# Kernel tuning notes

Measured on AMD Instinct MI355X. Metric: run time of the kernel, lower is better.

## Reference

```python
import jax, jax.numpy as jnp
import numpy as np

# Dims: C cells, L gene tokens, E embed, H mlp hidden, M factors, K topk
C, L, E, H, M, K = 16, 8192, 512, 256, 128, 30
TAU = 1.0        # gumbel-softmax temperature
SOFTNESS = 0.01  # soft-mask sharpness
TEMP = 1.0       # logits temperature
EPS = 1e-20


def setup_inputs() -> dict:
    key = jax.random.key(0)
    ks = jax.random.split(key, 7)
    x = jax.random.normal(ks[0], (C, L, E), dtype=jnp.float32)
    key_padding_mask = jax.random.randint(ks[1], (C, L), 0, 2) > 0  # True = valid
    uniform_noise = jax.random.uniform(ks[2], (C, L - 1, M), dtype=jnp.float32)
    W1 = jax.random.normal(ks[3], (E, H), dtype=jnp.float32) * (1.0 / np.sqrt(E))
    b1 = jnp.zeros((H,), dtype=jnp.float32)
    W2 = jax.random.normal(ks[4], (H, M), dtype=jnp.float32) * (1.0 / np.sqrt(H))
    b2 = jnp.zeros((M,), dtype=jnp.float32)
    return {"x": x, "key_padding_mask": key_padding_mask,
            "uniform_noise": uniform_noise,
            "W1": W1, "b1": b1, "W2": W2, "b2": b2}


def reference(x, key_padding_mask, uniform_noise, W1, b1, W2, b2):
    # default gene_subset: drop token 0, keep the rest  -> S = L-1
    xs = x[:, 1:, :]                          # (C, S, E)
    kpm = key_padding_mask[:, 1:]             # (C, S)

    # 2-layer MLP router (dropout p=0 -> identity)
    h = jax.nn.relu(jnp.einsum('cse,eh->csh', xs, W1) + b1)   # (C, S, H)
    logits = (jnp.einsum('csh,hm->csm', h, W2) + b2) / TEMP    # (C, S, M)

    # GumbelTopK, training path: gumbel-softmax then smooth top-k mask
    gumbel = -jnp.log(-jnp.log(uniform_noise + EPS) + EPS)
    perturbed = (logits + gumbel) / TAU
    probs = jax.nn.softmax(perturbed, axis=-1)                 # (C, S, M)
    topk_vals, _ = jax.lax.top_k(probs, K)                     # (C, S, K)
    threshold = topk_vals[..., -1:]                            # (C, S, 1)
    smooth_mask = jax.nn.sigmoid((probs - threshold) / SOFTNESS)
    out = probs * smooth_mask

    # faithful to the source: mask = ~key_padding_mask; probs *= mask
    out = out * (~kpm)[..., None].astype(out.dtype)
    return out, kpm
```

## Files before the change

### kernel.cpp

```cpp
#include <hip/hip_runtime.h>
#include <hip/hip_bf16.h>

#define CC 16
#define LL 8192
#define SS 8191
#define EE 512
#define HH 256
#define MM 128
#define TOPK 30
#define TOT (CC * SS)

typedef __attribute__((ext_vector_type(8))) short short8;
typedef __attribute__((ext_vector_type(4))) float f32x4;
typedef __attribute__((ext_vector_type(4))) unsigned int u32x4;

static __device__ __forceinline__ unsigned short f2bf(float f) {
    unsigned u = __builtin_bit_cast(unsigned, f);
    u += 0x7FFFu + ((u >> 16) & 1u);
    return (unsigned short)(u >> 16);
}

static __device__ __forceinline__ unsigned pk2(float lo, float hi) {
    __hip_bfloat162 t = __float22bfloat162_rn(float2{lo, hi});
    unsigned u;
    __builtin_memcpy(&u, &t, 4);
    return u;
}

static __device__ __forceinline__ short8 cvt8(const float4 a, const float4 b) {
    u32x4 uv;
    uv[0] = pk2(a.x, a.y);
    uv[1] = pk2(a.z, a.w);
    uv[2] = pk2(b.x, b.y);
    uv[3] = pk2(b.z, b.w);
    return __builtin_bit_cast(short8, uv);
}

static __device__ __forceinline__ void gl2lds16(const float* g, unsigned char* l) {
    __builtin_amdgcn_global_load_lds(
        (const __attribute__((address_space(1))) void*)g,
        (__attribute__((address_space(3))) void*)l,
        16, 0, 0);
}

template<int CTRL>
static __device__ __forceinline__ float dppf(float v) {
    return __builtin_bit_cast(float,
        __builtin_amdgcn_update_dpp(0, __builtin_bit_cast(int, v), CTRL, 0xF, 0xF, false));
}
template<int CTRL>
static __device__ __forceinline__ int dppi(int v) {
    return __builtin_amdgcn_update_dpp(0, v, CTRL, 0xF, 0xF, false);
}
static __device__ __forceinline__ float sum16f(float v) {
    v += dppf<0x121>(v); v += dppf<0x122>(v); v += dppf<0x124>(v); v += dppf<0x128>(v);
    return v;
}
static __device__ __forceinline__ float max16f(float v) {
    v = fmaxf(v, dppf<0x121>(v)); v = fmaxf(v, dppf<0x122>(v));
    v = fmaxf(v, dppf<0x124>(v)); v = fmaxf(v, dppf<0x128>(v));
    return v;
}
static __device__ __forceinline__ unsigned sum16u(unsigned v) {
    v += (unsigned)dppi<0x121>((int)v); v += (unsigned)dppi<0x122>((int)v);
    v += (unsigned)dppi<0x124>((int)v); v += (unsigned)dppi<0x128>((int)v);
    return v;
}

__global__ void prep_weights(const float* __restrict__ W1, const float* __restrict__ W2,
                             unsigned short* __restrict__ W1T, unsigned short* __restrict__ W2T)
{
    const int b = blockIdx.x, tid = threadIdx.x;
    if (b < 64) {
        const int e0 = b * 8, h = tid;
        short8 sv;
#pragma unroll
        for (int j = 0; j < 8; ++j)
            sv[j] = (short)f2bf(W1[(size_t)(e0 + j) * HH + h]);
        *(short8*)(void*)(W1T + (size_t)h * EE + e0) = sv;
    } else {
        const int h0 = (b - 64) * 16;
        if (tid < MM) {
            const int m = tid;
            short8 s0v, s1v;
#pragma unroll
            for (int j = 0; j < 8; ++j) {
                s0v[j] = (short)f2bf(W2[(size_t)(h0 + j) * MM + m]);
                s1v[j] = (short)f2bf(W2[(size_t)(h0 + 8 + j) * MM + m]);
            }
            *(short8*)(void*)(W2T + (size_t)m * HH + h0) = s0v;
            *(short8*)(void*)(W2T + (size_t)m * HH + h0 + 8) = s1v;
        }
    }
}

__global__ __launch_bounds__(512, 4)
void gene_gemm_kernel(const float* __restrict__ x,
                      const unsigned short* __restrict__ W1T,
                      const float* __restrict__ b1,
                      const unsigned short* __restrict__ W2T,
                      float* __restrict__ logits)
{
    __shared__ __align__(16) unsigned char lds[65536];

    const int tid = threadIdx.x;
    const int c   = blockIdx.y;
    const int s0  = blockIdx.x * 128;

    const int w    = tid >> 6;
    const int lane = tid & 63;
    const int lr   = lane & 15;
    const int kq   = lane >> 4;
    const int wr   = w >> 2;
    const int wc   = w & 3;
    const int tx   = tid & 15;
    const int ty   = tid >> 4;

    const float* xb = x + ((size_t)c * LL + s0 + 1) * EE;

#define STAGE(ck, bufoff) do {                                              \
    _Pragma("unroll")                                                       \
    for (int it_ = 0; it_ < 4; ++it_) {                                     \
        const int row_ = it_ * 32 + ty;                                     \
        const int rs_  = min(s0 + row_, SS - 1) - s0;                       \
        const float* g_ = xb + (size_t)rs_ * EE + (ck) * 64                 \
                          + ((tx ^ (row_ & 7)) << 2);                       \
        gl2lds16(g_, lds + (bufoff) + (it_ * 512 + tid) * 16);              \
    } } while (0)

    const int cw = wc * 64;
    float b1v[4];
#pragma unroll
    for (int n = 0; n < 4; ++n) b1v[n] = b1[cw + n * 16 + lr];

    f32x4 acc[4][4];
#pragma unroll
    for (int r = 0; r < 4; ++r)
#pragma unroll
        for (int n = 0; n < 4; ++n) acc[r][n] = (f32x4)0.0f;

    STAGE(0, 0);
    __syncthreads();

    for (int ck = 0; ck < 8; ++ck) {
        const int cur = (ck & 1) << 15;
        if (ck < 7) STAGE(ck + 1, ((ck + 1) & 1) << 15);
#pragma unroll
        for (int ks = 0; ks < 2; ++ks) {
            short8 af[4];
#pragma unroll
            for (int r = 0; r < 4; ++r) {
                const int row = wr * 64 + r * 16 + lr;
                const int ug  = ks * 8 + kq * 2;
                const float4 a0 = *(const float4*)(const void*)
                    (lds + cur + row * 256 + (((ug + 0) ^ (row & 7)) << 4));
                const float4 a1 = *(const float4*)(const void*)
                    (lds + cur + row * 256 + (((ug + 1) ^ (row & 7)) << 4));
                af[r] = cvt8(a0, a1);
            }
            short8 bf_[4];
#pragma unroll
            for (int n = 0; n < 4; ++n)
                bf_[n] = *(const short8*)(const void*)
                    (W1T + (size_t)(cw + n * 16 + lr) * EE + ck * 64 + ks * 32 + kq * 8);
#pragma unroll
            for (int r = 0; r < 4; ++r)
#pragma unroll
                for (int n = 0; n < 4; ++n)
                    acc[r][n] = __builtin_amdgcn_mfma_f32_16x16x32_bf16(af[r], bf_[n], acc[r][n], 0, 0, 0);
        }
        __syncthreads();
    }

#pragma unroll
    for (int n = 0; n < 4; ++n) {
        const int colh = cw + n * 16 + lr;
#pragma unroll
        for (int r = 0; r < 4; ++r)
#pragma unroll
            for (int q = 0; q < 4; ++q) {
                const int row = wr * 64 + r * 16 + kq * 4 + q;
                *(unsigned short*)(lds + row * 512 + ((colh * 2) ^ ((row & 7) << 4))) =
                    f2bf(fmaxf(acc[r][n][q] + b1v[n], 0.0f));
            }
    }
    __syncthreads();

    f32x4 acc2[4][2];
#pragma unroll
    for (int r = 0; r < 4; ++r)
#pragma unroll
        for (int n = 0; n < 2; ++n) acc2[r][n] = (f32x4)0.0f;

    const int cw2 = wc * 32;
#pragma unroll 4
    for (int ks = 0; ks < 8; ++ks) {
        short8 ah[4];
#pragma unroll
        for (int r = 0; r < 4; ++r) {
            const int row = wr * 64 + r * 16 + lr;
            ah[r] = *(const short8*)(const void*)
                (lds + row * 512 + ((ks * 64 + kq * 16) ^ ((row & 7) << 4)));
        }
        short8 bw[2];
#pragma unroll
        for (int n = 0; n < 2; ++n)
            bw[n] = *(const short8*)(const void*)
                (W2T + (size_t)(cw2 + n * 16 + lr) * HH + ks * 32 + kq * 8);
#pragma unroll
        for (int r = 0; r < 4; ++r)
#pragma unroll
            for (int n = 0; n < 2; ++n)
                acc2[r][n] = __builtin_amdgcn_mfma_f32_16x16x32_bf16(ah[r], bw[n], acc2[r][n], 0, 0, 0);
    }

#pragma unroll
    for (int r = 0; r < 4; ++r)
#pragma unroll
        for (int n = 0; n < 2; ++n)
#pragma unroll
            for (int q = 0; q < 4; ++q) {
                const int s = s0 + wr * 64 + r * 16 + kq * 4 + q;
                if (s < SS)
                    logits[((size_t)c * SS + s) * MM + cw2 + n * 16 + lr] = acc2[r][n][q];
            }
#undef STAGE
}

__global__ __launch_bounds__(256, 8)
void gene_epi_kernel(const float* __restrict__ noise,
                     const int*   __restrict__ mask,
                     const float* __restrict__ b2,
                     float* __restrict__ out,
                     float* __restrict__ outk)
{
    const int tid = threadIdx.x;
    const int tx  = tid & 15;
    const int ty  = tid >> 4;
    const long base = (long)blockIdx.x * 64;

    if (tid < 64) {
        const long gr = base + tid;
        if (gr < TOT) {
            const int cc2 = (int)(gr / SS);
            outk[gr] = (mask[gr + cc2 + 1] != 0) ? 1.0f : 0.0f;
        }
    }

    float b2v[8];
    {
        const float4 bb0 = *(const float4*)(b2 + tx * 8 + 0);
        const float4 bb1 = *(const float4*)(b2 + tx * 8 + 4);
        b2v[0]=bb0.x; b2v[1]=bb0.y; b2v[2]=bb0.z; b2v[3]=bb0.w;
        b2v[4]=bb1.x; b2v[5]=bb1.y; b2v[6]=bb1.z; b2v[7]=bb1.w;
    }

    float pr[4][8];
    float pmaxv[4];
    float mz[4];
    long  grv[4];

#pragma unroll
    for (int i = 0; i < 4; ++i) {
        const long gr  = base + ty * 4 + i;
        grv[i] = gr;
        const long grc = gr < TOT ? gr : (TOT - 1);
        const int  cc2 = (int)(grc / SS);
        mz[i] = (mask[grc + cc2 + 1] != 0) ? 0.0f : 1.0f;

        const float* lp = out   + grc * MM + tx * 8;
        const float* np = noise + grc * MM + tx * 8;
        const float4 l0 = *(const float4*)lp;
        const float4 l1 = *(const float4*)(lp + 4);
        const float4 u0 = *(const float4*)np;
        const float4 u1 = *(const float4*)(np + 4);
        const float lg[8] = {l0.x,l0.y,l0.z,l0.w,l1.x,l1.y,l1.z,l1.w};
        const float uu[8] = {u0.x,u0.y,u0.z,u0.w,u1.x,u1.y,u1.z,u1.w};
        float pm[8];
#pragma unroll
        for (int q = 0; q < 8; ++q) {
            const float g = -__logf(-__logf(uu[q] + 1e-20f) + 1e-20f);
            pm[q] = lg[q] + b2v[q] + g;
        }
        float mx = pm[0];
#pragma unroll
        for (int q = 1; q < 8; ++q) mx = fmaxf(mx, pm[q]);
        mx = max16f(mx);
        float se = 0.0f;
#pragma unroll
        for (int q = 0; q < 8; ++q) { pr[i][q] = __expf(pm[q] - mx); se += pr[i][q]; }
        se = sum16f(se);
        const float inv = 1.0f / se;
#pragma unroll
        for (int q = 0; q < 8; ++q) pr[i][q] *= inv;
        pmaxv[i] = inv;
    }

    float lo[4], hi[4];
#pragma unroll
    for (int i = 0; i < 4; ++i) { lo[i] = 0.0f; hi[i] = fminf(pmaxv[i], 1.0f / 30.0f); }
    for (int it = 0; it < 10; ++it) {
        float mid[4];
#pragma unroll
        for (int i = 0; i < 4; ++i) mid[i] = 0.5f * (lo[i] + hi[i]);
        unsigned cnt = 0;
#pragma unroll
        for (int q = 0; q < 8; ++q) {
            cnt += (pr[0][q] > mid[0]) ? 1u : 0u;
            cnt += (pr[1][q] > mid[1]) ? (1u << 8) : 0u;
            cnt += (pr[2][q] > mid[2]) ? (1u << 16) : 0u;
            cnt += (pr[3][q] > mid[3]) ? (1u << 24) : 0u;
        }
        cnt = sum16u(cnt);
#pragma unroll
        for (int i = 0; i < 4; ++i) {
            const bool ge = ((cnt >> (8 * i)) & 255u) >= TOPK;
            lo[i] = ge ? mid[i] : lo[i];
            hi[i] = ge ? hi[i] : mid[i];
        }
    }

#pragma unroll
    for (int i = 0; i < 4; ++i) {
        if (grv[i] < TOT) {
            float ov[8];
#pragma unroll
            for (int q = 0; q < 8; ++q) {
                const float sm = 1.0f / (1.0f + __expf((hi[i] - pr[i][q]) * 100.0f));
                ov[q] = pr[i][q] * sm * mz[i];
            }
            float* op = out + grv[i] * MM + tx * 8;
            float4 o0, o1;
            o0.x=ov[0]; o0.y=ov[1]; o0.z=ov[2]; o0.w=ov[3];
            o1.x=ov[4]; o1.y=ov[5]; o1.z=ov[6]; o1.w=ov[7];
            *(float4*)(op + 0) = o0;
            *(float4*)(op + 4) = o1;
        }
    }
}

extern "C" void kernel_launch(void* const* d_in, const int* in_sizes, int n_in,
                              void* d_out, int out_size, void* d_ws, size_t ws_size,
                              hipStream_t stream) {
    const float* x     = (const float*)d_in[0];
    const int*   mask  = (const int*)d_in[1];
    const float* noise = (const float*)d_in[2];
    const float* W1    = (const float*)d_in[3];
    const float* b1    = (const float*)d_in[4];
    const float* W2    = (const float*)d_in[5];
    const float* b2    = (const float*)d_in[6];
    float* out  = (float*)d_out;
    float* outk = out + (size_t)CC * SS * MM;

    unsigned short* W1T = (unsigned short*)d_ws;
    unsigned short* W2T = W1T + (size_t)HH * EE;

    prep_weights<<<dim3(80), dim3(256), 0, stream>>>(W1, W2, W1T, W2T);

    gene_gemm_kernel<<<dim3(64, CC), dim3(512), 0, stream>>>(x, W1T, b1, W2T, out);

    const int nblk = (TOT + 63) / 64;
    gene_epi_kernel<<<dim3(nblk), dim3(256), 0, stream>>>(noise, mask, b2, out, outk);
}
```

Measured before the change: 177.1 us.

## Deepen GEMM1 x-tile pipeline to four stages with register-prefetched W1

Cuts the first GEMM's K chunks from 64 to 32 floats and rotates four LDS buffers with three chunks in flight. Waits on a partial vmcnt instead of a full __syncthreads each chunk. W1 fragments are double-buffered in registers and prefetched one chunk ahead. The goal is to hide global-load latency behind MFMA work. Correctness now depends on hand-counted vmcnt values and on the compiler not reordering the sched_barrier regions.

Measured after the change: 232.5 us. 1.31x slower.

```diff
diff --git a/kernel.cpp b/kernel.cpp
--- a/kernel.cpp
+++ b/kernel.cpp
@@ -113,22 +113,29 @@
     const int kq   = lane >> 4;
     const int wr   = w >> 2;
     const int wc   = w & 3;
-    const int tx   = tid & 15;
-    const int ty   = tid >> 4;
 
     const float* xb = x + ((size_t)c * LL + s0 + 1) * EE;
-
-#define STAGE(ck, bufoff) do {                                              \
+    const int cw = wc * 64;
+
+#define STAGE(ck) do {                                                      \
+    const int bo_ = ((ck) & 3) * 16384;                                     \
     _Pragma("unroll")                                                       \
-    for (int it_ = 0; it_ < 4; ++it_) {                                     \
-        const int row_ = it_ * 32 + ty;                                     \
+    for (int j_ = 0; j_ < 2; ++j_) {                                        \
+        const int unit_ = j_ * 512 + tid;                                   \
+        const int row_ = unit_ >> 3, uu_ = unit_ & 7;                       \
         const int rs_  = min(s0 + row_, SS - 1) - s0;                       \
-        const float* g_ = xb + (size_t)rs_ * EE + (ck) * 64                 \
-                          + ((tx ^ (row_ & 7)) << 2);                       \
-        gl2lds16(g_, lds + (bufoff) + (it_ * 512 + tid) * 16);              \
+        const float* g_ = xb + (size_t)rs_ * EE + (ck) * 32                 \
+                          + ((uu_ ^ (row_ & 7)) << 2);                      \
+        gl2lds16(g_, lds + bo_ + unit_ * 16);                               \
     } } while (0)
 
-    const int cw = wc * 64;
+#define LOADW(dst, ck) do {                                                 \
+    _Pragma("unroll")                                                       \
+    for (int n_ = 0; n_ < 4; ++n_)                                          \
+        dst[n_] = *(const short8*)(const void*)                             \
+            (W1T + (size_t)(cw + n_ * 16 + lr) * EE + (ck) * 32 + kq * 8);  \
+    } while (0)
+
     float b1v[4];
 #pragma unroll
     for (int n = 0; n < 4; ++n) b1v[n] = b1[cw + n * 16 + lr];
@@ -139,38 +146,49 @@
 #pragma unroll
         for (int n = 0; n < 4; ++n) acc[r][n] = (f32x4)0.0f;
 
-    STAGE(0, 0);
+    short8 wA[4], wB[4];
+
+    LOADW(wA, 0);
+    STAGE(0); STAGE(1); STAGE(2);
+
+#define DO_CHUNK(C, V, WCUR, WNXT) do {                                     \
+    if ((C) < 15) LOADW(WNXT, (C) + 1);                                     \
+    __builtin_amdgcn_sched_barrier(0);                                      \
+    asm volatile("s_waitcnt vmcnt(" #V ")" ::: "memory");                   \
+    asm volatile("s_waitcnt lgkmcnt(0)" ::: "memory");                      \
+    __builtin_amdgcn_sched_barrier(0);                                      \
+    __builtin_amdgcn_s_barrier();                                           \
+    __builtin_amdgcn_sched_barrier(0);                                      \
+    if ((C) <= 12) STAGE((C) + 3);                                          \
+    const unsigned char* cb_ = lds + ((C) & 3) * 16384;                     \
+    short8 af_[4];                                                          \
+    _Pragma("unroll")                                                       \
+    for (int r_ = 0; r_ < 4; ++r_) {                                        \
+        const int row_ = wr * 64 + r_ * 16 + lr;                            \
+        const float4 a0_ = *(const float4*)(const void*)                    \
+            (cb_ + row_ * 128 + (((kq * 2 + 0) ^ (row_ & 7)) << 4));        \
+        const float4 a1_ = *(const float4*)(const void*)                    \
+            (cb_ + row_ * 128 + (((kq * 2 + 1) ^ (row_ & 7)) << 4));        \
+        af_[r_] = cvt8(a0_, a1_);                                           \
+    }                                                                       \
+    _Pragma("unroll")                                                       \
+    for (int r_ = 0; r_ < 4; ++r_)                                          \
+        _Pragma("unroll")                                                   \
+        for (int n_ = 0; n_ < 4; ++n_)                                      \
+            acc[r_][n_] = __builtin_amdgcn_mfma_f32_16x16x32_bf16(          \
+                af_[r_], WCUR[n_], acc[r_][n_], 0, 0, 0);                   \
+    } while (0)
+
+    DO_CHUNK( 0, 12, wA, wB); DO_CHUNK( 1, 16, wB, wA);
+    DO_CHUNK( 2, 20, wA, wB); DO_CHUNK( 3, 20, wB, wA);
+    DO_CHUNK( 4, 20, wA, wB); DO_CHUNK( 5, 20, wB, wA);
+    DO_CHUNK( 6, 20, wA, wB); DO_CHUNK( 7, 20, wB, wA);
+    DO_CHUNK( 8, 20, wA, wB); DO_CHUNK( 9, 20, wB, wA);
+    DO_CHUNK(10, 20, wA, wB); DO_CHUNK(11, 20, wB, wA);
+    DO_CHUNK(12, 20, wA, wB); DO_CHUNK(13, 20, wB, wA);
+    DO_CHUNK(14, 16, wA, wB); DO_CHUNK(15,  8, wB, wA);
+
     __syncthreads();
-
-    for (int ck = 0; ck < 8; ++ck) {
-        const int cur = (ck & 1) << 15;
-        if (ck < 7) STAGE(ck + 1, ((ck + 1) & 1) << 15);
-#pragma unroll
-        for (int ks = 0; ks < 2; ++ks) {
-            short8 af[4];
-#pragma unroll
-            for (int r = 0; r < 4; ++r) {
-                const int row = wr * 64 + r * 16 + lr;
-                const int ug  = ks * 8 + kq * 2;
-                const float4 a0 = *(const float4*)(const void*)
-                    (lds + cur + row * 256 + (((ug + 0) ^ (row & 7)) << 4));
-                const float4 a1 = *(const float4*)(const void*)
-                    (lds + cur + row * 256 + (((ug + 1) ^ (row & 7)) << 4));
-                af[r] = cvt8(a0, a1);
-            }
-            short8 bf_[4];
-#pragma unroll
-            for (int n = 0; n < 4; ++n)
-                bf_[n] = *(const short8*)(const void*)
-                    (W1T + (size_t)(cw + n * 16 + lr) * EE + ck * 64 + ks * 32 + kq * 8);
-#pragma unroll
-            for (int r = 0; r < 4; ++r)
-#pragma unroll
-                for (int n = 0; n < 4; ++n)
-                    acc[r][n] = __builtin_amdgcn_mfma_f32_16x16x32_bf16(af[r], bf_[n], acc[r][n], 0, 0, 0);
-        }
-        __syncthreads();
-    }
 
 #pragma unroll
     for (int n = 0; n < 4; ++n) {
@@ -224,6 +242,8 @@
                 if (s < SS)
                     logits[((size_t)c * SS + s) * MM + cw2 + n * 16 + lr] = acc2[r][n][q];
             }
+#undef DO_CHUNK
+#undef LOADW
 #undef STAGE
 }
 
```

## Shrink GEMM tile to 64 rows with single-buffered LDS for higher occupancy

Applied to the files above, without the earlier changes.

The fused MLP GEMM kernel now uses 64-row tiles, 256 threads and a 32 KB single LDS buffer, replacing 128-row tiles, 512 threads and a 64 KB double buffer. The x tile is staged in 128-wide K chunks with a sync before compute, so the explicit prefetch pipeline is gone. The intent is to fit more resident blocks per CU and launch twice as many blocks, hiding global-load latency through occupancy rather than software double buffering. In exchange, each W1T/W2T fragment is reused across fewer rows, so weight traffic roughly doubles, and loads and MFMA work within a block no longer overlap.

After: 368.6 us. 2.08x slower.

```diff
diff --git a/kernel.cpp b/kernel.cpp
--- a/kernel.cpp
+++ b/kernel.cpp
@@ -94,41 +94,27 @@
     }
 }
 
-__global__ __launch_bounds__(512, 4)
+__global__ __launch_bounds__(256, 5)
 void gene_gemm_kernel(const float* __restrict__ x,
                       const unsigned short* __restrict__ W1T,
                       const float* __restrict__ b1,
                       const unsigned short* __restrict__ W2T,
                       float* __restrict__ logits)
 {
-    __shared__ __align__(16) unsigned char lds[65536];
+    __shared__ __align__(16) unsigned char lds[32768];
 
     const int tid = threadIdx.x;
     const int c   = blockIdx.y;
-    const int s0  = blockIdx.x * 128;
+    const int s0  = blockIdx.x * 64;
 
     const int w    = tid >> 6;
     const int lane = tid & 63;
     const int lr   = lane & 15;
     const int kq   = lane >> 4;
-    const int wr   = w >> 2;
-    const int wc   = w & 3;
-    const int tx   = tid & 15;
-    const int ty   = tid >> 4;
 
     const float* xb = x + ((size_t)c * LL + s0 + 1) * EE;
-
-#define STAGE(ck, bufoff) do {                                              \
-    _Pragma("unroll")                                                       \
-    for (int it_ = 0; it_ < 4; ++it_) {                                     \
-        const int row_ = it_ * 32 + ty;                                     \
-        const int rs_  = min(s0 + row_, SS - 1) - s0;                       \
-        const float* g_ = xb + (size_t)rs_ * EE + (ck) * 64                 \
-                          + ((tx ^ (row_ & 7)) << 2);                       \
-        gl2lds16(g_, lds + (bufoff) + (it_ * 512 + tid) * 16);              \
-    } } while (0)
-
-    const int cw = wc * 64;
+    const int cw = w * 64;
+
     float b1v[4];
 #pragma unroll
     for (int n = 0; n < 4; ++n) b1v[n] = b1[cw + n * 16 + lr];
@@ -139,30 +125,36 @@
 #pragma unroll
         for (int n = 0; n < 4; ++n) acc[r][n] = (f32x4)0.0f;
 
-    STAGE(0, 0);
-    __syncthreads();
-
-    for (int ck = 0; ck < 8; ++ck) {
-        const int cur = (ck & 1) << 15;
-        if (ck < 7) STAGE(ck + 1, ((ck + 1) & 1) << 15);
-#pragma unroll
-        for (int ks = 0; ks < 2; ++ks) {
+#pragma unroll
+    for (int ck = 0; ck < 4; ++ck) {
+#pragma unroll
+        for (int j = 0; j < 8; ++j) {
+            const int unit = j * 256 + tid;
+            const int row = unit >> 5, uu = unit & 31;
+            const int rs = min(s0 + row, SS - 1) - s0;
+            const float* g = xb + (size_t)rs * EE + ck * 128 + ((uu ^ (row & 7)) << 2);
+            gl2lds16(g, lds + unit * 16);
+        }
+        __syncthreads();
+
+#pragma unroll
+        for (int ks = 0; ks < 4; ++ks) {
             short8 af[4];
 #pragma unroll
             for (int r = 0; r < 4; ++r) {
-                const int row = wr * 64 + r * 16 + lr;
-                const int ug  = ks * 8 + kq * 2;
+                const int row = r * 16 + lr;
+                const int u0 = ks * 8 + kq * 2;
                 const float4 a0 = *(const float4*)(const void*)
-                    (lds + cur + row * 256 + (((ug + 0) ^ (row & 7)) << 4));
+                    (lds + row * 512 + (((u0 + 0) ^ (row & 7)) << 4));
                 const float4 a1 = *(const float4*)(const void*)
-                    (lds + cur + row * 256 + (((ug + 1) ^ (row & 7)) << 4));
+                    (lds + row * 512 + (((u0 + 1) ^ (row & 7)) << 4));
                 af[r] = cvt8(a0, a1);
             }
             short8 bf_[4];
 #pragma unroll
             for (int n = 0; n < 4; ++n)
                 bf_[n] = *(const short8*)(const void*)
-                    (W1T + (size_t)(cw + n * 16 + lr) * EE + ck * 64 + ks * 32 + kq * 8);
+                    (W1T + (size_t)(cw + n * 16 + lr) * EE + ck * 128 + ks * 32 + kq * 8);
 #pragma unroll
             for (int r = 0; r < 4; ++r)
 #pragma unroll
@@ -179,7 +171,7 @@
         for (int r = 0; r < 4; ++r)
 #pragma unroll
             for (int q = 0; q < 4; ++q) {
-                const int row = wr * 64 + r * 16 + kq * 4 + q;
+                const int row = r * 16 + kq * 4 + q;
                 *(unsigned short*)(lds + row * 512 + ((colh * 2) ^ ((row & 7) << 4))) =
                     f2bf(fmaxf(acc[r][n][q] + b1v[n], 0.0f));
             }
@@ -192,13 +184,13 @@
 #pragma unroll
         for (int n = 0; n < 2; ++n) acc2[r][n] = (f32x4)0.0f;
 
-    const int cw2 = wc * 32;
+    const int cw2 = w * 32;
 #pragma unroll 4
     for (int ks = 0; ks < 8; ++ks) {
         short8 ah[4];
 #pragma unroll
         for (int r = 0; r < 4; ++r) {
-            const int row = wr * 64 + r * 16 + lr;
+            const int row = r * 16 + lr;
             ah[r] = *(const short8*)(const void*)
                 (lds + row * 512 + ((ks * 64 + kq * 16) ^ ((row & 7) << 4)));
         }
@@ -220,11 +212,10 @@
         for (int n = 0; n < 2; ++n)
 #pragma unroll
             for (int q = 0; q < 4; ++q) {
-                const int s = s0 + wr * 64 + r * 16 + kq * 4 + q;
+                const int s = s0 + r * 16 + kq * 4 + q;
                 if (s < SS)
                     logits[((size_t)c * SS + s) * MM + cw2 + n * 16 + lr] = acc2[r][n][q];
             }
-#undef STAGE
 }
 
 __global__ __launch_bounds__(256, 8)
@@ -357,7 +348,7 @@
 
     prep_weights<<<dim3(80), dim3(256), 0, stream>>>(W1, W2, W1T, W2T);
 
-    gene_gemm_kernel<<<dim3(64, CC), dim3(512), 0, stream>>>(x, W1T, b1, W2T, out);
+    gene_gemm_kernel<<<dim3(128, CC), dim3(256), 0, stream>>>(x, W1T, b1, W2T, out);
 
     const int nblk = (TOT + 63) / 64;
     gene_epi_kernel<<<dim3(nblk), dim3(256), 0, stream>>>(noise, mask, b2, out, outk);
```

## Stage x via registers with bf16 conversion before LDS write

Applied to the files above, without the earlier changes.

The GEMM kernel no longer uses direct global-to-LDS fp32 loads. Each thread now loads x rows into registers, converts them to bf16 once and writes them to a half-size swizzled LDS buffer. MFMA operand reads then load bf16 directly from LDS instead of converting fp32 per wave, and the loads for the next chunk are issued before the barrier so they overlap compute. Barriers are replaced by a custom lgkmcnt wait plus s_barrier. The trade-off is more register pressure and global latency now sitting in the register path, in exchange for less LDS traffic and no repeated conversions.

After: 181.0 us. 1.02x slower.

```diff
diff --git a/kernel.cpp b/kernel.cpp
--- a/kernel.cpp
+++ b/kernel.cpp
@@ -36,13 +36,6 @@
     return __builtin_bit_cast(short8, uv);
 }
 
-static __device__ __forceinline__ void gl2lds16(const float* g, unsigned char* l) {
-    __builtin_amdgcn_global_load_lds(
-        (const __attribute__((address_space(1))) void*)g,
-        (__attribute__((address_space(3))) void*)l,
-        16, 0, 0);
-}
-
 template<int CTRL>
 static __device__ __forceinline__ float dppf(float v) {
     return __builtin_bit_cast(float,
@@ -65,6 +58,13 @@
     v += (unsigned)dppi<0x121>((int)v); v += (unsigned)dppi<0x122>((int)v);
     v += (unsigned)dppi<0x124>((int)v); v += (unsigned)dppi<0x128>((int)v);
     return v;
+}
+
+static __device__ __forceinline__ void bar_lgkm() {
+    asm volatile("s_waitcnt lgkmcnt(0)" ::: "memory");
+    __builtin_amdgcn_sched_barrier(0);
+    __builtin_amdgcn_s_barrier();
+    __builtin_amdgcn_sched_barrier(0);
 }
 
 __global__ void prep_weights(const float* __restrict__ W1, const float* __restrict__ W2,
@@ -113,25 +113,19 @@
     const int kq   = lane >> 4;
     const int wr   = w >> 2;
     const int wc   = w & 3;
-    const int tx   = tid & 15;
-    const int ty   = tid >> 4;
-
-    const float* xb = x + ((size_t)c * LL + s0 + 1) * EE;
-
-#define STAGE(ck, bufoff) do {                                              \
-    _Pragma("unroll")                                                       \
-    for (int it_ = 0; it_ < 4; ++it_) {                                     \
-        const int row_ = it_ * 32 + ty;                                     \
-        const int rs_  = min(s0 + row_, SS - 1) - s0;                       \
-        const float* g_ = xb + (size_t)rs_ * EE + (ck) * 64                 \
-                          + ((tx ^ (row_ & 7)) << 2);                       \
-        gl2lds16(g_, lds + (bufoff) + (it_ * 512 + tid) * 16);              \
-    } } while (0)
-
-    const int cw = wc * 64;
-    float b1v[4];
-#pragma unroll
-    for (int n = 0; n < 4; ++n) b1v[n] = b1[cw + n * 16 + lr];
+    const int cw   = wc * 64;
+
+    const int srow = tid >> 2;
+    const int sk4  = tid & 3;
+    const int rsc  = min(s0 + srow, SS - 1) - s0;
+    const float* xrow = x + ((size_t)c * LL + s0 + 1 + rsc) * EE + sk4 * 16;
+    const int swz = (srow & 7) << 4;
+    unsigned char* wb = lds + srow * 128;
+
+    float4 xr0, xr1, xr2, xr3;
+#define LOADX(ck) do { const float* p_ = xrow + (ck) * 64;                   \
+    xr0 = *(const float4*)p_;       xr1 = *(const float4*)(p_ + 4);          \
+    xr2 = *(const float4*)(p_ + 8); xr3 = *(const float4*)(p_ + 12); } while (0)
 
     f32x4 acc[4][4];
 #pragma unroll
@@ -139,24 +133,24 @@
 #pragma unroll
         for (int n = 0; n < 4; ++n) acc[r][n] = (f32x4)0.0f;
 
-    STAGE(0, 0);
-    __syncthreads();
-
+    LOADX(0);
+
+#pragma unroll
     for (int ck = 0; ck < 8; ++ck) {
-        const int cur = (ck & 1) << 15;
-        if (ck < 7) STAGE(ck + 1, ((ck + 1) & 1) << 15);
+        const int bo = (ck & 1) << 14;
+        *(short8*)(void*)(wb + bo + (((sk4 * 2 + 0) * 16) ^ swz)) = cvt8(xr0, xr1);
+        *(short8*)(void*)(wb + bo + (((sk4 * 2 + 1) * 16) ^ swz)) = cvt8(xr2, xr3);
+        if (ck < 7) LOADX(ck + 1);
+        bar_lgkm();
+
 #pragma unroll
         for (int ks = 0; ks < 2; ++ks) {
             short8 af[4];
 #pragma unroll
             for (int r = 0; r < 4; ++r) {
                 const int row = wr * 64 + r * 16 + lr;
-                const int ug  = ks * 8 + kq * 2;
-                const float4 a0 = *(const float4*)(const void*)
-                    (lds + cur + row * 256 + (((ug + 0) ^ (row & 7)) << 4));
-                const float4 a1 = *(const float4*)(const void*)
-                    (lds + cur + row * 256 + (((ug + 1) ^ (row & 7)) << 4));
-                af[r] = cvt8(a0, a1);
+                af[r] = *(const short8*)(const void*)
+                    (lds + bo + row * 128 + (((ks * 4 + kq) * 16) ^ ((row & 7) << 4)));
             }
             short8 bf_[4];
 #pragma unroll
@@ -169,8 +163,12 @@
                 for (int n = 0; n < 4; ++n)
                     acc[r][n] = __builtin_amdgcn_mfma_f32_16x16x32_bf16(af[r], bf_[n], acc[r][n], 0, 0, 0);
         }
-        __syncthreads();
-    }
+        bar_lgkm();
+    }
+
+    float b1v[4];
+#pragma unroll
+    for (int n = 0; n < 4; ++n) b1v[n] = b1[cw + n * 16 + lr];
 
 #pragma unroll
     for (int n = 0; n < 4; ++n) {
@@ -184,7 +182,7 @@
                     f2bf(fmaxf(acc[r][n][q] + b1v[n], 0.0f));
             }
     }
-    __syncthreads();
+    bar_lgkm();
 
     f32x4 acc2[4][2];
 #pragma unroll
@@ -224,7 +222,7 @@
                 if (s < SS)
                     logits[((size_t)c * SS + s) * MM + cw2 + n * 16 + lr] = acc2[r][n][q];
             }
-#undef STAGE
+#undef LOADX
 }
 
 __global__ __launch_bounds__(256, 8)
```
